# Kernel tuning notes

Hardware: AMD Instinct MI355X
Metric: run time of the kernel (lower is better)

## Reference

```python
import jax, jax.numpy as jnp
import numpy as np

EPS = 1e-5  # nn.BatchNorm1d default eps


def setup_inputs() -> dict:
    key = jax.random.key(0)
    k1, k2, k3 = jax.random.split(key, 3)
    B, N, Fin, Fout = 16, 8192, 256, 256
    x = jax.random.normal(k1, (B, N, Fin), dtype=jnp.float32)
    # nn.Linear init: U(-1/sqrt(in), 1/sqrt(in))
    bound = 1.0 / np.sqrt(Fin)
    W = jax.random.uniform(k2, (Fout, Fin), dtype=jnp.float32, minval=-bound, maxval=bound)
    b = jax.random.uniform(k3, (Fout,), dtype=jnp.float32, minval=-bound, maxval=bound)
    gamma = jnp.ones((Fout,), dtype=jnp.float32)   # BatchNorm1d weight
    beta = jnp.zeros((Fout,), dtype=jnp.float32)   # BatchNorm1d bias
    return {"x": x, "W": W, "b": b, "gamma": gamma, "beta": beta}


def reference(x, W, b, gamma, beta):
    # Linear: [B, N, Fin] @ [Fin, Fout] + b -> [B, N, Fout]
    y = jnp.einsum("bnf,of->bno", x, W) + b
    # Per-sample BatchNorm1d (training mode): stats over N (axis=1) per feature,
    # biased variance, shared affine params. Vectorized over the batch loop.
    mean = jnp.mean(y, axis=1, keepdims=True)              # [B, 1, Fout]
    var = jnp.mean((y - mean) ** 2, axis=1, keepdims=True)  # biased var [B, 1, Fout]
    y_hat = (y - mean) * jax.lax.rsqrt(var + EPS)
    return y_hat * gamma + beta
```

## Files before the change

kernel.cpp:

```cpp
#include <hip/hip_runtime.h>
#include <hip/hip_bf16.h>


typedef __attribute__((ext_vector_type(8))) __bf16 bf16x8;
typedef __attribute__((ext_vector_type(4))) float f32x4;
typedef __attribute__((ext_vector_type(8))) unsigned short ushort8;

#define BDIM   16
#define NDIM   8192
#define FIN    256
#define FOUT   256
#define BM     128
#define BN     128
#define BKSTEP 64
#define NTHREADS 256

__device__ __forceinline__ void split_pack(const float4 v0, const float4 v1,
                                           ushort8& h, ushort8& l) {
  float f[8] = {v0.x, v0.y, v0.z, v0.w, v1.x, v1.y, v1.z, v1.w};
#pragma unroll
  for (int i = 0; i < 8; ++i) {
    unsigned int u  = __float_as_uint(f[i]);
    unsigned int hu = u & 0xFFFF0000u;
    h[i] = (unsigned short)(u >> 16);
    float rem = f[i] - __uint_as_float(hu);
    l[i] = (unsigned short)(__float_as_uint(rem) >> 16);
  }
}

template <int MODE>
__global__ __launch_bounds__(NTHREADS, 2)
void fused_gemm(const float* __restrict__ X, const float* __restrict__ W,
                float* __restrict__ Y,
                float* __restrict__ P1, float* __restrict__ P2,
                const float* __restrict__ Sc, const float* __restrict__ Tc) {
  __shared__ __align__(16) char lds[65536];
  char* Abh = lds;
  char* Abl = lds + 16384;
  char* Bbh = lds + 32768;
  char* Bbl = lds + 49152;

  const int tid  = threadIdx.x;
  const int rblk = blockIdx.x;
  const int cblk = blockIdx.y;
  const size_t rowBase = (size_t)rblk * BM;
  const int colBase = cblk * BN;

  const int wid  = tid >> 6;
  const int lane = tid & 63;
  const int wr   = wid >> 1;
  const int wc   = wid & 1;
  const int lg   = lane >> 4;
  const int lr   = lane & 15;

  f32x4 acc[4][4];
#pragma unroll
  for (int m = 0; m < 4; ++m)
#pragma unroll
    for (int n = 0; n < 4; ++n) acc[m][n] = f32x4{0.f, 0.f, 0.f, 0.f};

  for (int ks = 0; ks < FIN / BKSTEP; ++ks) {
    const int k0 = ks * BKSTEP;
#pragma unroll
    for (int c = 0; c < 4; ++c) {
      int id = tid + c * NTHREADS;
      int r  = id >> 3;
      int kc = id & 7;
      int boff = r * 128 + ((kc * 16) ^ ((r & 7) << 4));
      {
        const float4* ga = (const float4*)(X + (rowBase + r) * (size_t)FIN + k0 + kc * 8);
        ushort8 h, l;
        split_pack(ga[0], ga[1], h, l);
        *(ushort8*)(Abh + boff) = h;
        *(ushort8*)(Abl + boff) = l;
      }
      {
        const float4* gb = (const float4*)(W + (size_t)(colBase + r) * FIN + k0 + kc * 8);
        ushort8 h, l;
        split_pack(gb[0], gb[1], h, l);
        *(ushort8*)(Bbh + boff) = h;
        *(ushort8*)(Bbl + boff) = l;
      }
    }
    __syncthreads();
#pragma unroll
    for (int kk = 0; kk < 2; ++kk) {
      bf16x8 ah[4], al[4], bh[4], bl[4];
#pragma unroll
      for (int m = 0; m < 4; ++m) {
        int row  = wr * 64 + m * 16 + lr;
        int boff = row * 128 + ((kk * 64 + lg * 16) ^ ((row & 7) << 4));
        ah[m] = *(const bf16x8*)(Abh + boff);
        al[m] = *(const bf16x8*)(Abl + boff);
      }
#pragma unroll
      for (int n = 0; n < 4; ++n) {
        int row  = wc * 64 + n * 16 + lr;
        int boff = row * 128 + ((kk * 64 + lg * 16) ^ ((row & 7) << 4));
        bh[n] = *(const bf16x8*)(Bbh + boff);
        bl[n] = *(const bf16x8*)(Bbl + boff);
      }
#pragma unroll
      for (int m = 0; m < 4; ++m)
#pragma unroll
        for (int n = 0; n < 4; ++n) {
          acc[m][n] = __builtin_amdgcn_mfma_f32_16x16x32_bf16(ah[m], bh[n], acc[m][n], 0, 0, 0);
          acc[m][n] = __builtin_amdgcn_mfma_f32_16x16x32_bf16(ah[m], bl[n], acc[m][n], 0, 0, 0);
          acc[m][n] = __builtin_amdgcn_mfma_f32_16x16x32_bf16(al[m], bh[n], acc[m][n], 0, 0, 0);
        }
    }
    __syncthreads();
  }

  if (MODE == 0) {
#pragma unroll
    for (int m = 0; m < 4; ++m) {
      size_t row = rowBase + wr * 64 + m * 16 + lg * 4;
#pragma unroll
      for (int n = 0; n < 4; ++n) {
        int col = colBase + wc * 64 + n * 16 + lr;
#pragma unroll
        for (int r = 0; r < 4; ++r)
          Y[(row + r) * (size_t)FOUT + col] = acc[m][n][r];
      }
    }
  }

  if (MODE <= 1) {
    float ps1[4], ps2[4];
#pragma unroll
    for (int n = 0; n < 4; ++n) {
      ps1[n] = 0.f; ps2[n] = 0.f;
#pragma unroll
      for (int m = 0; m < 4; ++m)
#pragma unroll
        for (int r = 0; r < 4; ++r) {
          float v = acc[m][n][r];
          ps1[n] += v; ps2[n] += v * v;
        }
      ps1[n] += __shfl_xor(ps1[n], 16);
      ps1[n] += __shfl_xor(ps1[n], 32);
      ps2[n] += __shfl_xor(ps2[n], 16);
      ps2[n] += __shfl_xor(ps2[n], 32);
    }
    __syncthreads();
    float* red = (float*)lds;
    if (lr == lane) {}
    if (lane < 16) {
#pragma unroll
      for (int n = 0; n < 4; ++n) {
        red[wid * 64 + n * 16 + lr]       = ps1[n];
        red[256 + wid * 64 + n * 16 + lr] = ps2[n];
      }
    }
    __syncthreads();
    if (tid < 128) {
      int ccb = tid >> 6, cc = tid & 63;
      float s1 = red[ccb * 64 + cc] + red[(2 + ccb) * 64 + cc];
      float s2 = red[256 + ccb * 64 + cc] + red[256 + (2 + ccb) * 64 + cc];
      P1[(size_t)rblk * FOUT + colBase + tid] = s1;
      P2[(size_t)rblk * FOUT + colBase + tid] = s2;
    }
  }

  if (MODE == 2) {
    const int b = rblk >> 6;
#pragma unroll
    for (int n = 0; n < 4; ++n) {
      int col  = colBase + wc * 64 + n * 16 + lr;
      float sc = Sc[b * FOUT + col];
      float tc = Tc[b * FOUT + col];
#pragma unroll
      for (int m = 0; m < 4; ++m) {
        size_t row = rowBase + wr * 64 + m * 16 + lg * 4;
#pragma unroll
        for (int r = 0; r < 4; ++r)
          Y[(row + r) * (size_t)FOUT + col] = fmaf(acc[m][n][r], sc, tc);
      }
    }
  }
}

__global__ void reduce_stats(const float* __restrict__ P1, const float* __restrict__ P2,
                             const float* __restrict__ gamma, const float* __restrict__ beta,
                             float* __restrict__ Sc, float* __restrict__ Tc) {
  int t = blockIdx.x * blockDim.x + threadIdx.x;
  int b = t >> 8, o = t & 255;
  float s1 = 0.f, s2 = 0.f;
  for (int r = 0; r < 64; ++r) {
    size_t idx = ((size_t)(b * 64 + r)) * FOUT + o;
    s1 += P1[idx];
    s2 += P2[idx];
  }
  float mean = s1 * (1.f / (float)NDIM);
  float var  = s2 * (1.f / (float)NDIM) - mean * mean;
  float rstd = rsqrtf(var + 1e-5f);
  float g    = gamma[o] * rstd;
  Sc[t] = g;
  Tc[t] = beta[o] - mean * g;
}

__global__ void normalize_y(const float4* __restrict__ Yv,
                            const float* __restrict__ Sc, const float* __restrict__ Tc,
                            float4* __restrict__ Ov) {
  const int total = (BDIM * NDIM * FOUT) / 4;
  for (int i = blockIdx.x * blockDim.x + threadIdx.x; i < total;
       i += gridDim.x * blockDim.x) {
    float4 y = Yv[i];
    size_t e = (size_t)i * 4;
    int o = (int)(e & 255);
    int b = (int)(e >> 21);
    const float4 s = *(const float4*)(Sc + b * 256 + o);
    const float4 t = *(const float4*)(Tc + b * 256 + o);
    float4 r;
    r.x = fmaf(y.x, s.x, t.x);
    r.y = fmaf(y.y, s.y, t.y);
    r.z = fmaf(y.z, s.z, t.z);
    r.w = fmaf(y.w, s.w, t.w);
    Ov[i] = r;
  }
}

extern "C" void kernel_launch(void* const* d_in, const int* in_sizes, int n_in,
                              void* d_out, int out_size, void* d_ws, size_t ws_size,
                              hipStream_t stream) {
  const float* X     = (const float*)d_in[0];
  const float* W     = (const float*)d_in[1];
  const float* gamma = (const float*)d_in[3];
  const float* beta  = (const float*)d_in[4];
  float* out = (float*)d_out;
  float* wsf = (float*)d_ws;

  const size_t yElems = (size_t)BDIM * NDIM * FOUT;
  const size_t pElems = 1024u * FOUT;
  const size_t needA  = (yElems + 2 * pElems + 2 * 4096) * sizeof(float);

  dim3 grid(1024, 2), blk(NTHREADS);
  if (ws_size >= needA) {
    float* Y  = wsf;
    float* P1 = wsf + yElems;
    float* P2 = P1 + pElems;
    float* Sc = P2 + pElems;
    float* Tc = Sc + 4096;
    fused_gemm<0><<<grid, blk, 0, stream>>>(X, W, Y, P1, P2, nullptr, nullptr);
    reduce_stats<<<16, 256, 0, stream>>>(P1, P2, gamma, beta, Sc, Tc);
    normalize_y<<<2048, 256, 0, stream>>>((const float4*)Y, Sc, Tc, (float4*)out);
  } else {
    float* P1 = wsf;
    float* P2 = P1 + pElems;
    float* Sc = P2 + pElems;
    float* Tc = Sc + 4096;
    fused_gemm<1><<<grid, blk, 0, stream>>>(X, W, nullptr, P1, P2, nullptr, nullptr);
    reduce_stats<<<16, 256, 0, stream>>>(P1, P2, gamma, beta, Sc, Tc);
    fused_gemm<2><<<grid, blk, 0, stream>>>(X, W, out, P1, P2, Sc, Tc);
  }
}
```

Baseline: 322.0 us.

## Pre-split W into bf16 hi/lo, halve column tile, transpose partial stats

A small kernel now splits W into bf16 high and low parts once per call. The GEMM reads B fragments straight from global memory instead of staging them in LDS, which halves LDS use. The column tile shrinks to 64 and launch bounds allow 4 blocks per CU, so occupancy should rise. The partial column sums are stored transposed, so reduce_stats can do one wave-per-output shuffle reduction over many blocks. The trade-off is that each X tile is now loaded and split four times instead of twice, roughly doubling X global traffic and conversion work.

```diff
diff --git a/kernel.cpp b/kernel.cpp
--- a/kernel.cpp
+++ b/kernel.cpp
@@ -4,41 +4,60 @@
 
 typedef __attribute__((ext_vector_type(8))) __bf16 bf16x8;
 typedef __attribute__((ext_vector_type(4))) float f32x4;
-typedef __attribute__((ext_vector_type(8))) unsigned short ushort8;
+typedef __attribute__((ext_vector_type(8))) unsigned short us8;
+typedef __attribute__((ext_vector_type(4))) unsigned short us4;
 
 #define BDIM   16
 #define NDIM   8192
 #define FIN    256
 #define FOUT   256
 #define BM     128
-#define BN     128
-#define BKSTEP 64
+#define BN     64
+#define BK     64
 #define NTHREADS 256
-
-__device__ __forceinline__ void split_pack(const float4 v0, const float4 v1,
-                                           ushort8& h, ushort8& l) {
+#define NRBLK  (BDIM * NDIM / BM)
+#define NCBLK  (FOUT / BN)
+
+__device__ __forceinline__ void split8(const float4 v0, const float4 v1,
+                                       us8& h, us8& l) {
   float f[8] = {v0.x, v0.y, v0.z, v0.w, v1.x, v1.y, v1.z, v1.w};
 #pragma unroll
   for (int i = 0; i < 8; ++i) {
-    unsigned int u  = __float_as_uint(f[i]);
-    unsigned int hu = u & 0xFFFF0000u;
+    unsigned int u = __float_as_uint(f[i]);
     h[i] = (unsigned short)(u >> 16);
-    float rem = f[i] - __uint_as_float(hu);
+    float rem = f[i] - __uint_as_float(u & 0xFFFF0000u);
     l[i] = (unsigned short)(__float_as_uint(rem) >> 16);
   }
 }
 
+__global__ void split_w(const float4* __restrict__ Wv,
+                        us4* __restrict__ Wh, us4* __restrict__ Wl) {
+  int gid = blockIdx.x * blockDim.x + threadIdx.x;
+  float4 v = Wv[gid];
+  float f[4] = {v.x, v.y, v.z, v.w};
+  us4 h, l;
+#pragma unroll
+  for (int i = 0; i < 4; ++i) {
+    unsigned int u = __float_as_uint(f[i]);
+    h[i] = (unsigned short)(u >> 16);
+    float rem = f[i] - __uint_as_float(u & 0xFFFF0000u);
+    l[i] = (unsigned short)(__float_as_uint(rem) >> 16);
+  }
+  Wh[gid] = h;
+  Wl[gid] = l;
+}
+
 template <int MODE>
-__global__ __launch_bounds__(NTHREADS, 2)
-void fused_gemm(const float* __restrict__ X, const float* __restrict__ W,
+__global__ __launch_bounds__(NTHREADS, 4)
+void fused_gemm(const float* __restrict__ X,
+                const unsigned short* __restrict__ Wh,
+                const unsigned short* __restrict__ Wl,
                 float* __restrict__ Y,
                 float* __restrict__ P1, float* __restrict__ P2,
                 const float* __restrict__ Sc, const float* __restrict__ Tc) {
-  __shared__ __align__(16) char lds[65536];
+  __shared__ __align__(16) char lds[2 * BM * BK * 2];
   char* Abh = lds;
-  char* Abl = lds + 16384;
-  char* Bbh = lds + 32768;
-  char* Bbl = lds + 49152;
+  char* Abl = lds + BM * BK * 2;
 
   const int tid  = threadIdx.x;
   const int rblk = blockIdx.x;
@@ -46,46 +65,36 @@
   const size_t rowBase = (size_t)rblk * BM;
   const int colBase = cblk * BN;
 
-  const int wid  = tid >> 6;
-  const int lane = tid & 63;
-  const int wr   = wid >> 1;
-  const int wc   = wid & 1;
-  const int lg   = lane >> 4;
-  const int lr   = lane & 15;
-
-  f32x4 acc[4][4];
+  const int wid = tid >> 6, lane = tid & 63;
+  const int wr = wid >> 1, wc = wid & 1;
+  const int lg = lane >> 4, lr = lane & 15;
+
+  f32x4 acc[4][2];
 #pragma unroll
   for (int m = 0; m < 4; ++m)
 #pragma unroll
-    for (int n = 0; n < 4; ++n) acc[m][n] = f32x4{0.f, 0.f, 0.f, 0.f};
-
-  for (int ks = 0; ks < FIN / BKSTEP; ++ks) {
-    const int k0 = ks * BKSTEP;
+    for (int n = 0; n < 2; ++n) acc[m][n] = f32x4{0.f, 0.f, 0.f, 0.f};
+
+  for (int ks = 0; ks < FIN / BK; ++ks) {
+    const int k0 = ks * BK;
 #pragma unroll
     for (int c = 0; c < 4; ++c) {
       int id = tid + c * NTHREADS;
       int r  = id >> 3;
       int kc = id & 7;
+      const float4* ga =
+          (const float4*)(X + (rowBase + r) * (size_t)FIN + k0 + kc * 8);
+      float4 v0 = ga[0], v1 = ga[1];
+      us8 h, l;
+      split8(v0, v1, h, l);
       int boff = r * 128 + ((kc * 16) ^ ((r & 7) << 4));
-      {
-        const float4* ga = (const float4*)(X + (rowBase + r) * (size_t)FIN + k0 + kc * 8);
-        ushort8 h, l;
-        split_pack(ga[0], ga[1], h, l);
-        *(ushort8*)(Abh + boff) = h;
-        *(ushort8*)(Abl + boff) = l;
-      }
-      {
-        const float4* gb = (const float4*)(W + (size_t)(colBase + r) * FIN + k0 + kc * 8);
-        ushort8 h, l;
-        split_pack(gb[0], gb[1], h, l);
-        *(ushort8*)(Bbh + boff) = h;
-        *(ushort8*)(Bbl + boff) = l;
-      }
+      *(us8*)(Abh + boff) = h;
+      *(us8*)(Abl + boff) = l;
     }
     __syncthreads();
 #pragma unroll
     for (int kk = 0; kk < 2; ++kk) {
-      bf16x8 ah[4], al[4], bh[4], bl[4];
+      bf16x8 ah[4], al[4];
 #pragma unroll
       for (int m = 0; m < 4; ++m) {
         int row  = wr * 64 + m * 16 + lr;
@@ -94,20 +103,18 @@
         al[m] = *(const bf16x8*)(Abl + boff);
       }
 #pragma unroll
-      for (int n = 0; n < 4; ++n) {
-        int row  = wc * 64 + n * 16 + lr;
-        int boff = row * 128 + ((kk * 64 + lg * 16) ^ ((row & 7) << 4));
-        bh[n] = *(const bf16x8*)(Bbh + boff);
-        bl[n] = *(const bf16x8*)(Bbl + boff);
-      }
-#pragma unroll
-      for (int m = 0; m < 4; ++m)
-#pragma unroll
-        for (int n = 0; n < 4; ++n) {
-          acc[m][n] = __builtin_amdgcn_mfma_f32_16x16x32_bf16(ah[m], bh[n], acc[m][n], 0, 0, 0);
-          acc[m][n] = __builtin_amdgcn_mfma_f32_16x16x32_bf16(ah[m], bl[n], acc[m][n], 0, 0, 0);
-          acc[m][n] = __builtin_amdgcn_mfma_f32_16x16x32_bf16(al[m], bh[n], acc[m][n], 0, 0, 0);
+      for (int n = 0; n < 2; ++n) {
+        int col = colBase + wc * 32 + n * 16 + lr;
+        size_t woff = (size_t)col * FIN + k0 + kk * 32 + lg * 8;
+        bf16x8 bh = *(const bf16x8*)(Wh + woff);
+        bf16x8 bl = *(const bf16x8*)(Wl + woff);
+#pragma unroll
+        for (int m = 0; m < 4; ++m) {
+          acc[m][n] = __builtin_amdgcn_mfma_f32_16x16x32_bf16(ah[m], bh, acc[m][n], 0, 0, 0);
+          acc[m][n] = __builtin_amdgcn_mfma_f32_16x16x32_bf16(ah[m], bl, acc[m][n], 0, 0, 0);
+          acc[m][n] = __builtin_amdgcn_mfma_f32_16x16x32_bf16(al[m], bh, acc[m][n], 0, 0, 0);
         }
+      }
     }
     __syncthreads();
   }
@@ -117,8 +124,8 @@
     for (int m = 0; m < 4; ++m) {
       size_t row = rowBase + wr * 64 + m * 16 + lg * 4;
 #pragma unroll
-      for (int n = 0; n < 4; ++n) {
-        int col = colBase + wc * 64 + n * 16 + lr;
+      for (int n = 0; n < 2; ++n) {
+        int col = colBase + wc * 32 + n * 16 + lr;
 #pragma unroll
         for (int r = 0; r < 4; ++r)
           Y[(row + r) * (size_t)FOUT + col] = acc[m][n][r];
@@ -127,9 +134,9 @@
   }
 
   if (MODE <= 1) {
-    float ps1[4], ps2[4];
-#pragma unroll
-    for (int n = 0; n < 4; ++n) {
+    float ps1[2], ps2[2];
+#pragma unroll
+    for (int n = 0; n < 2; ++n) {
       ps1[n] = 0.f; ps2[n] = 0.f;
 #pragma unroll
       for (int m = 0; m < 4; ++m)
@@ -145,29 +152,28 @@
     }
     __syncthreads();
     float* red = (float*)lds;
-    if (lr == lane) {}
     if (lane < 16) {
 #pragma unroll
-      for (int n = 0; n < 4; ++n) {
-        red[wid * 64 + n * 16 + lr]       = ps1[n];
-        red[256 + wid * 64 + n * 16 + lr] = ps2[n];
-      }
-    }
-    __syncthreads();
-    if (tid < 128) {
-      int ccb = tid >> 6, cc = tid & 63;
-      float s1 = red[ccb * 64 + cc] + red[(2 + ccb) * 64 + cc];
-      float s2 = red[256 + ccb * 64 + cc] + red[256 + (2 + ccb) * 64 + cc];
-      P1[(size_t)rblk * FOUT + colBase + tid] = s1;
-      P2[(size_t)rblk * FOUT + colBase + tid] = s2;
+      for (int n = 0; n < 2; ++n) {
+        red[wid * 32 + n * 16 + lr]       = ps1[n];
+        red[128 + wid * 32 + n * 16 + lr] = ps2[n];
+      }
+    }
+    __syncthreads();
+    if (tid < BN) {
+      int c = tid, j = c & 31, wb = c >> 5;
+      float s1 = red[wb * 32 + j] + red[(wb + 2) * 32 + j];
+      float s2 = red[128 + wb * 32 + j] + red[128 + (wb + 2) * 32 + j];
+      P1[(size_t)(colBase + c) * NRBLK + rblk] = s1;
+      P2[(size_t)(colBase + c) * NRBLK + rblk] = s2;
     }
   }
 
   if (MODE == 2) {
     const int b = rblk >> 6;
 #pragma unroll
-    for (int n = 0; n < 4; ++n) {
-      int col  = colBase + wc * 64 + n * 16 + lr;
+    for (int n = 0; n < 2; ++n) {
+      int col  = colBase + wc * 32 + n * 16 + lr;
       float sc = Sc[b * FOUT + col];
       float tc = Tc[b * FOUT + col];
 #pragma unroll
@@ -184,20 +190,24 @@
 __global__ void reduce_stats(const float* __restrict__ P1, const float* __restrict__ P2,
                              const float* __restrict__ gamma, const float* __restrict__ beta,
                              float* __restrict__ Sc, float* __restrict__ Tc) {
-  int t = blockIdx.x * blockDim.x + threadIdx.x;
-  int b = t >> 8, o = t & 255;
-  float s1 = 0.f, s2 = 0.f;
-  for (int r = 0; r < 64; ++r) {
-    size_t idx = ((size_t)(b * 64 + r)) * FOUT + o;
-    s1 += P1[idx];
-    s2 += P2[idx];
-  }
-  float mean = s1 * (1.f / (float)NDIM);
-  float var  = s2 * (1.f / (float)NDIM) - mean * mean;
-  float rstd = rsqrtf(var + 1e-5f);
-  float g    = gamma[o] * rstd;
-  Sc[t] = g;
-  Tc[t] = beta[o] - mean * g;
+  int p = blockIdx.x * 4 + (threadIdx.x >> 6);
+  int lane = threadIdx.x & 63;
+  int b = p >> 8, o = p & 255;
+  size_t base = (size_t)o * NRBLK + b * 64;
+  float s1 = P1[base + lane];
+  float s2 = P2[base + lane];
+#pragma unroll
+  for (int off = 32; off; off >>= 1) {
+    s1 += __shfl_xor(s1, off);
+    s2 += __shfl_xor(s2, off);
+  }
+  if (lane == 0) {
+    float mean = s1 * (1.f / (float)NDIM);
+    float var  = s2 * (1.f / (float)NDIM) - mean * mean;
+    float g    = gamma[o] * rsqrtf(var + 1e-5f);
+    Sc[p] = g;
+    Tc[p] = beta[o] - mean * g;
+  }
 }
 
 __global__ void normalize_y(const float4* __restrict__ Yv,
@@ -232,26 +242,33 @@
   float* wsf = (float*)d_ws;
 
   const size_t yElems = (size_t)BDIM * NDIM * FOUT;
-  const size_t pElems = 1024u * FOUT;
-  const size_t needA  = (yElems + 2 * pElems + 2 * 4096) * sizeof(float);
-
-  dim3 grid(1024, 2), blk(NTHREADS);
+  const size_t pElems = (size_t)FOUT * NRBLK;
+  const size_t whFloats = (FOUT * FIN) / 2;
+  const size_t needA = (yElems + 2 * pElems + 2 * 4096 + 2 * whFloats) * sizeof(float);
+
+  dim3 grid(NRBLK, NCBLK), blk(NTHREADS);
   if (ws_size >= needA) {
     float* Y  = wsf;
     float* P1 = wsf + yElems;
     float* P2 = P1 + pElems;
     float* Sc = P2 + pElems;
     float* Tc = Sc + 4096;
-    fused_gemm<0><<<grid, blk, 0, stream>>>(X, W, Y, P1, P2, nullptr, nullptr);
-    reduce_stats<<<16, 256, 0, stream>>>(P1, P2, gamma, beta, Sc, Tc);
-    normalize_y<<<2048, 256, 0, stream>>>((const float4*)Y, Sc, Tc, (float4*)out);
+    unsigned short* Wh = (unsigned short*)(Tc + 4096);
+    unsigned short* Wl = Wh + FOUT * FIN;
+    split_w<<<64, 256, 0, stream>>>((const float4*)W, (us4*)Wh, (us4*)Wl);
+    fused_gemm<0><<<grid, blk, 0, stream>>>(X, Wh, Wl, Y, P1, P2, nullptr, nullptr);
+    reduce_stats<<<1024, 256, 0, stream>>>(P1, P2, gamma, beta, Sc, Tc);
+    normalize_y<<<4096, 256, 0, stream>>>((const float4*)Y, Sc, Tc, (float4*)out);
   } else {
     float* P1 = wsf;
     float* P2 = P1 + pElems;
     float* Sc = P2 + pElems;
     float* Tc = Sc + 4096;
-    fused_gemm<1><<<grid, blk, 0, stream>>>(X, W, nullptr, P1, P2, nullptr, nullptr);
-    reduce_stats<<<16, 256, 0, stream>>>(P1, P2, gamma, beta, Sc, Tc);
-    fused_gemm<2><<<grid, blk, 0, stream>>>(X, W, out, P1, P2, Sc, Tc);
-  }
-}
+    unsigned short* Wh = (unsigned short*)(Tc + 4096);
+    unsigned short* Wl = Wh + FOUT * FIN;
+    split_w<<<64, 256, 0, stream>>>((const float4*)W, (us4*)Wh, (us4*)Wl);
+    fused_gemm<1><<<grid, blk, 0, stream>>>(X, Wh, Wl, nullptr, P1, P2, nullptr, nullptr);
+    reduce_stats<<<1024, 256, 0, stream>>>(P1, P2, gamma, beta, Sc, Tc);
+    fused_gemm<2><<<grid, blk, 0, stream>>>(X, Wh, Wl, out, P1, P2, Sc, Tc);
+  }
+}
```

Measured after the change: 365.3 us. 13.4% more time.

## Pre-split X and W into swizzled bf16 hi/lo tiles and load via LDS DMA

Applied to the files above, without the earlier changes.

Adds separate kernels that split X and W into bf16 high/low halves stored in the GEMM's swizzled tile layout, so the GEMM loads tiles straight into LDS with global_load_lds instead of converting in-kernel. It also transposes the partial-stat layout and rewrites reduce_stats as a wave-shuffle reduction. This removes conversion ALU work and register staging from the GEMM's inner loop, at the cost of an extra full pass over X plus a 128 MB write of hi/lo data.

```diff
diff --git a/kernel.cpp b/kernel.cpp
--- a/kernel.cpp
+++ b/kernel.cpp
@@ -4,7 +4,7 @@
 
 typedef __attribute__((ext_vector_type(8))) __bf16 bf16x8;
 typedef __attribute__((ext_vector_type(4))) float f32x4;
-typedef __attribute__((ext_vector_type(8))) unsigned short ushort8;
+typedef __attribute__((ext_vector_type(8))) unsigned short us8;
 
 #define BDIM   16
 #define NDIM   8192
@@ -12,25 +12,78 @@
 #define FOUT   256
 #define BM     128
 #define BN     128
-#define BKSTEP 64
-#define NTHREADS 256
-
-__device__ __forceinline__ void split_pack(const float4 v0, const float4 v1,
-                                           ushort8& h, ushort8& l) {
+#define BK     64
+#define NTH    256
+#define NRBLK  1024
+#define NCBLK  2
+#define NKS    4
+#define TILEB  16384
+
+__device__ __forceinline__ int swz(int r, int c) {
+  return r * 128 + ((c * 16) ^ ((r & 7) << 4));
+}
+
+__device__ __forceinline__ void split8(const float4 v0, const float4 v1,
+                                       us8& h, us8& l) {
   float f[8] = {v0.x, v0.y, v0.z, v0.w, v1.x, v1.y, v1.z, v1.w};
 #pragma unroll
   for (int i = 0; i < 8; ++i) {
-    unsigned int u  = __float_as_uint(f[i]);
-    unsigned int hu = u & 0xFFFF0000u;
+    unsigned int u = __float_as_uint(f[i]);
     h[i] = (unsigned short)(u >> 16);
-    float rem = f[i] - __uint_as_float(hu);
+    float rem = f[i] - __uint_as_float(u & 0xFFFF0000u);
     l[i] = (unsigned short)(__float_as_uint(rem) >> 16);
   }
 }
 
+__device__ __forceinline__ void gload_lds16(const void* g, void* l) {
+  __builtin_amdgcn_global_load_lds(
+      (const __attribute__((address_space(1))) unsigned int*)g,
+      (__attribute__((address_space(3))) unsigned int*)l, 16, 0, 0);
+}
+
+__global__ void split_x(const float* __restrict__ X,
+                        unsigned short* __restrict__ Xh,
+                        unsigned short* __restrict__ Xl) {
+  const int total = (BDIM * NDIM) * (FIN / 8);
+  for (int i = blockIdx.x * blockDim.x + threadIdx.x; i < total;
+       i += gridDim.x * blockDim.x) {
+    int row = i >> 5;
+    int rem = i & 31;
+    int ks = rem >> 3, c = rem & 7;
+    const float4* g = (const float4*)(X + (size_t)row * FIN + ks * BK + c * 8);
+    float4 v0 = g[0], v1 = g[1];
+    us8 h, l;
+    split8(v0, v1, h, l);
+    size_t tb = ((size_t)(row >> 7) * NKS + ks) * TILEB;
+    int boff = swz(row & 127, c);
+    *(us8*)((char*)Xh + tb + boff) = h;
+    *(us8*)((char*)Xl + tb + boff) = l;
+  }
+}
+
+__global__ void split_w(const float* __restrict__ W,
+                        unsigned short* __restrict__ Wh,
+                        unsigned short* __restrict__ Wl) {
+  int i = blockIdx.x * blockDim.x + threadIdx.x;
+  int row = i >> 5;
+  int rem = i & 31;
+  int ks = rem >> 3, c = rem & 7;
+  const float4* g = (const float4*)(W + (size_t)row * FIN + ks * BK + c * 8);
+  float4 v0 = g[0], v1 = g[1];
+  us8 h, l;
+  split8(v0, v1, h, l);
+  size_t tb = ((size_t)(row >> 7) * NKS + ks) * TILEB;
+  int boff = swz(row & 127, c);
+  *(us8*)((char*)Wh + tb + boff) = h;
+  *(us8*)((char*)Wl + tb + boff) = l;
+}
+
 template <int MODE>
-__global__ __launch_bounds__(NTHREADS, 2)
-void fused_gemm(const float* __restrict__ X, const float* __restrict__ W,
+__global__ __launch_bounds__(NTH, 2)
+void fused_gemm(const unsigned short* __restrict__ Xh,
+                const unsigned short* __restrict__ Xl,
+                const unsigned short* __restrict__ Wh,
+                const unsigned short* __restrict__ Wl,
                 float* __restrict__ Y,
                 float* __restrict__ P1, float* __restrict__ P2,
                 const float* __restrict__ Sc, const float* __restrict__ Tc) {
@@ -43,15 +96,9 @@
   const int tid  = threadIdx.x;
   const int rblk = blockIdx.x;
   const int cblk = blockIdx.y;
-  const size_t rowBase = (size_t)rblk * BM;
-  const int colBase = cblk * BN;
-
-  const int wid  = tid >> 6;
-  const int lane = tid & 63;
-  const int wr   = wid >> 1;
-  const int wc   = wid & 1;
-  const int lg   = lane >> 4;
-  const int lr   = lane & 15;
+  const int wid = tid >> 6, lane = tid & 63;
+  const int wr = wid >> 1, wc = wid & 1;
+  const int lg = lane >> 4, lr = lane & 15;
 
   f32x4 acc[4][4];
 #pragma unroll
@@ -59,28 +106,21 @@
 #pragma unroll
     for (int n = 0; n < 4; ++n) acc[m][n] = f32x4{0.f, 0.f, 0.f, 0.f};
 
-  for (int ks = 0; ks < FIN / BKSTEP; ++ks) {
-    const int k0 = ks * BKSTEP;
-#pragma unroll
-    for (int c = 0; c < 4; ++c) {
-      int id = tid + c * NTHREADS;
-      int r  = id >> 3;
-      int kc = id & 7;
-      int boff = r * 128 + ((kc * 16) ^ ((r & 7) << 4));
-      {
-        const float4* ga = (const float4*)(X + (rowBase + r) * (size_t)FIN + k0 + kc * 8);
-        ushort8 h, l;
-        split_pack(ga[0], ga[1], h, l);
-        *(ushort8*)(Abh + boff) = h;
-        *(ushort8*)(Abl + boff) = l;
-      }
-      {
-        const float4* gb = (const float4*)(W + (size_t)(colBase + r) * FIN + k0 + kc * 8);
-        ushort8 h, l;
-        split_pack(gb[0], gb[1], h, l);
-        *(ushort8*)(Bbh + boff) = h;
-        *(ushort8*)(Bbl + boff) = l;
-      }
+  const char* gAh = (const char*)Xh + (size_t)rblk * NKS * TILEB;
+  const char* gAl = (const char*)Xl + (size_t)rblk * NKS * TILEB;
+  const char* gBh = (const char*)Wh + (size_t)cblk * NKS * TILEB;
+  const char* gBl = (const char*)Wl + (size_t)cblk * NKS * TILEB;
+
+  for (int ks = 0; ks < NKS; ++ks) {
+    const size_t kb = (size_t)ks * TILEB;
+#pragma unroll
+    for (int j = 0; j < 4; ++j) {
+      int so = (wid * 4 + j) * 1024;
+      int go = so + lane * 16;
+      gload_lds16(gAh + kb + go, Abh + so);
+      gload_lds16(gAl + kb + go, Abl + so);
+      gload_lds16(gBh + kb + go, Bbh + so);
+      gload_lds16(gBl + kb + go, Bbl + so);
     }
     __syncthreads();
 #pragma unroll
@@ -88,15 +128,13 @@
       bf16x8 ah[4], al[4], bh[4], bl[4];
 #pragma unroll
       for (int m = 0; m < 4; ++m) {
-        int row  = wr * 64 + m * 16 + lr;
-        int boff = row * 128 + ((kk * 64 + lg * 16) ^ ((row & 7) << 4));
+        int boff = swz(wr * 64 + m * 16 + lr, kk * 4 + lg);
         ah[m] = *(const bf16x8*)(Abh + boff);
         al[m] = *(const bf16x8*)(Abl + boff);
       }
 #pragma unroll
       for (int n = 0; n < 4; ++n) {
-        int row  = wc * 64 + n * 16 + lr;
-        int boff = row * 128 + ((kk * 64 + lg * 16) ^ ((row & 7) << 4));
+        int boff = swz(wc * 64 + n * 16 + lr, kk * 4 + lg);
         bh[n] = *(const bf16x8*)(Bbh + boff);
         bl[n] = *(const bf16x8*)(Bbl + boff);
       }
@@ -111,6 +149,9 @@
     }
     __syncthreads();
   }
+
+  const size_t rowBase = (size_t)rblk * BM;
+  const int colBase = cblk * BN;
 
   if (MODE == 0) {
 #pragma unroll
@@ -145,7 +186,6 @@
     }
     __syncthreads();
     float* red = (float*)lds;
-    if (lr == lane) {}
     if (lane < 16) {
 #pragma unroll
       for (int n = 0; n < 4; ++n) {
@@ -154,12 +194,12 @@
       }
     }
     __syncthreads();
-    if (tid < 128) {
-      int ccb = tid >> 6, cc = tid & 63;
-      float s1 = red[ccb * 64 + cc] + red[(2 + ccb) * 64 + cc];
-      float s2 = red[256 + ccb * 64 + cc] + red[256 + (2 + ccb) * 64 + cc];
-      P1[(size_t)rblk * FOUT + colBase + tid] = s1;
-      P2[(size_t)rblk * FOUT + colBase + tid] = s2;
+    if (tid < BN) {
+      int wcs = tid >> 6, j = tid & 63;
+      float s1 = red[wcs * 64 + j] + red[(2 + wcs) * 64 + j];
+      float s2 = red[256 + wcs * 64 + j] + red[256 + (2 + wcs) * 64 + j];
+      P1[(size_t)(colBase + tid) * NRBLK + rblk] = s1;
+      P2[(size_t)(colBase + tid) * NRBLK + rblk] = s2;
     }
   }
 
@@ -184,20 +224,24 @@
 __global__ void reduce_stats(const float* __restrict__ P1, const float* __restrict__ P2,
                              const float* __restrict__ gamma, const float* __restrict__ beta,
                              float* __restrict__ Sc, float* __restrict__ Tc) {
-  int t = blockIdx.x * blockDim.x + threadIdx.x;
-  int b = t >> 8, o = t & 255;
-  float s1 = 0.f, s2 = 0.f;
-  for (int r = 0; r < 64; ++r) {
-    size_t idx = ((size_t)(b * 64 + r)) * FOUT + o;
-    s1 += P1[idx];
-    s2 += P2[idx];
-  }
-  float mean = s1 * (1.f / (float)NDIM);
-  float var  = s2 * (1.f / (float)NDIM) - mean * mean;
-  float rstd = rsqrtf(var + 1e-5f);
-  float g    = gamma[o] * rstd;
-  Sc[t] = g;
-  Tc[t] = beta[o] - mean * g;
+  int p = blockIdx.x * 4 + (threadIdx.x >> 6);
+  int lane = threadIdx.x & 63;
+  int b = p >> 8, o = p & 255;
+  size_t base = (size_t)o * NRBLK + b * 64;
+  float s1 = P1[base + lane];
+  float s2 = P2[base + lane];
+#pragma unroll
+  for (int off = 32; off; off >>= 1) {
+    s1 += __shfl_xor(s1, off);
+    s2 += __shfl_xor(s2, off);
+  }
+  if (lane == 0) {
+    float mean = s1 * (1.f / (float)NDIM);
+    float var  = s2 * (1.f / (float)NDIM) - mean * mean;
+    float g    = gamma[o] * rsqrtf(var + 1e-5f);
+    Sc[p] = g;
+    Tc[p] = beta[o] - mean * g;
+  }
 }
 
 __global__ void normalize_y(const float4* __restrict__ Yv,
@@ -229,29 +273,46 @@
   const float* gamma = (const float*)d_in[3];
   const float* beta  = (const float*)d_in[4];
   float* out = (float*)d_out;
-  float* wsf = (float*)d_ws;
-
-  const size_t yElems = (size_t)BDIM * NDIM * FOUT;
-  const size_t pElems = 1024u * FOUT;
-  const size_t needA  = (yElems + 2 * pElems + 2 * 4096) * sizeof(float);
-
-  dim3 grid(1024, 2), blk(NTHREADS);
+  char* ws = (char*)d_ws;
+
+  const size_t yB  = (size_t)BDIM * NDIM * FOUT * 4;
+  const size_t pB  = (size_t)FOUT * NRBLK * 4;
+  const size_t scB = 4096 * 4;
+  const size_t wB  = (size_t)FOUT * FIN * 2;
+  const size_t xB  = (size_t)BDIM * NDIM * FIN * 2;
+
+  const size_t needAp = 2 * pB + 2 * scB + 2 * wB + 2 * xB;
+  const size_t needA  = needAp + yB;
+
+  dim3 grid(NRBLK, NCBLK), blk(NTH);
   if (ws_size >= needA) {
-    float* Y  = wsf;
-    float* P1 = wsf + yElems;
-    float* P2 = P1 + pElems;
-    float* Sc = P2 + pElems;
-    float* Tc = Sc + 4096;
-    fused_gemm<0><<<grid, blk, 0, stream>>>(X, W, Y, P1, P2, nullptr, nullptr);
-    reduce_stats<<<16, 256, 0, stream>>>(P1, P2, gamma, beta, Sc, Tc);
-    normalize_y<<<2048, 256, 0, stream>>>((const float4*)Y, Sc, Tc, (float4*)out);
+    float* Y  = (float*)ws;
+    float* P1 = (float*)(ws + yB);
+    float* P2 = (float*)(ws + yB + pB);
+    float* Sc = (float*)(ws + yB + 2 * pB);
+    float* Tc = (float*)(ws + yB + 2 * pB + scB);
+    unsigned short* Wh = (unsigned short*)(ws + yB + 2 * pB + 2 * scB);
+    unsigned short* Wl = (unsigned short*)(ws + yB + 2 * pB + 2 * scB + wB);
+    unsigned short* Xh = (unsigned short*)(ws + yB + 2 * pB + 2 * scB + 2 * wB);
+    unsigned short* Xl = (unsigned short*)(ws + yB + 2 * pB + 2 * scB + 2 * wB + xB);
+    split_w<<<32, 256, 0, stream>>>(W, Wh, Wl);
+    split_x<<<2048, 256, 0, stream>>>(X, Xh, Xl);
+    fused_gemm<0><<<grid, blk, 0, stream>>>(Xh, Xl, Wh, Wl, Y, P1, P2, nullptr, nullptr);
+    reduce_stats<<<1024, 256, 0, stream>>>(P1, P2, gamma, beta, Sc, Tc);
+    normalize_y<<<4096, 256, 0, stream>>>((const float4*)Y, Sc, Tc, (float4*)out);
   } else {
-    float* P1 = wsf;
-    float* P2 = P1 + pElems;
-    float* Sc = P2 + pElems;
-    float* Tc = Sc + 4096;
-    fused_gemm<1><<<grid, blk, 0, stream>>>(X, W, nullptr, P1, P2, nullptr, nullptr);
-    reduce_stats<<<16, 256, 0, stream>>>(P1, P2, gamma, beta, Sc, Tc);
-    fused_gemm<2><<<grid, blk, 0, stream>>>(X, W, out, P1, P2, Sc, Tc);
-  }
-}
+    float* P1 = (float*)ws;
+    float* P2 = (float*)(ws + pB);
+    float* Sc = (float*)(ws + 2 * pB);
+    float* Tc = (float*)(ws + 2 * pB + scB);
+    unsigned short* Wh = (unsigned short*)(ws + 2 * pB + 2 * scB);
+    unsigned short* Wl = (unsigned short*)(ws + 2 * pB + 2 * scB + wB);
+    unsigned short* Xh = (unsigned short*)(ws + 2 * pB + 2 * scB + 2 * wB);
+    unsigned short* Xl = (unsigned short*)(ws + 2 * pB + 2 * scB + 2 * wB + xB);
+    split_w<<<32, 256, 0, stream>>>(W, Wh, Wl);
+    split_x<<<2048, 256, 0, stream>>>(X, Xh, Xl);
+    fused_gemm<1><<<grid, blk, 0, stream>>>(Xh, Xl, Wh, Wl, nullptr, P1, P2, nullptr, nullptr);
+    reduce_stats<<<1024, 256, 0, stream>>>(P1, P2, gamma, beta, Sc, Tc);
+    fused_gemm<2><<<grid, blk, 0, stream>>>(Xh, Xl, Wh, Wl, out, P1, P2, Sc, Tc);
+  }
+}
```

Measured after the change: 378.4 us. 17.5% more time.
